# Kernel tuning notes

Measured on AMD Instinct MI355X. Metric: run time of the kernel, lower is better.

Reference implementation:

```python
import jax, jax.numpy as jnp
import numpy as np

GROUP = 5  # in-group size implied by `expected_in = indices.shape[1] * 5`


def setup_inputs() -> dict:
    key = jax.random.key(0)
    k1, k2, k3, k4 = jax.random.split(key, 4)
    T, IN, OUT, G, C, K = 64, 4100, 12288, 820, 2, 256
    x = jax.random.normal(k1, (T, IN), dtype=jnp.float32)
    indices = jax.random.randint(k2, (OUT, G, C), 0, K, dtype=jnp.int32)
    codebooks = (jax.random.normal(k3, (C, K, GROUP), dtype=jnp.float32) * 0.05).astype(jnp.float16)
    scales = jax.random.uniform(k4, (OUT,), dtype=jnp.float32, minval=0.5, maxval=1.5)
    return {"x": x, "indices": indices, "codebooks": codebooks, "scales": scales}


def reference(x, indices, codebooks, scales):
    orig_shape = x.shape
    x_flat = x.reshape(-1, orig_shape[-1])
    expected_in = indices.shape[1] * GROUP
    pad = expected_in - x_flat.shape[1]
    if pad > 0:
        x_flat = jnp.pad(x_flat, ((0, 0), (0, pad)))
    # safety scaling (fp16 overflow guard), as in the torch module
    x_max = jnp.maximum(jnp.abs(x_flat).max(), 1.0) * 8.0
    cb_max = jnp.maximum(jnp.abs(codebooks).astype(jnp.float32).max(), 1.0)
    x_safe = (x_flat / x_max).astype(jnp.float16)
    cb_safe = (codebooks.astype(jnp.float32) / cb_max).astype(jnp.float16)
    # additive-codebook dequant: W[o, g] = sum_c cb_safe[c, indices[o,g,c], :]
    C = cb_safe.shape[0]
    gathered = cb_safe[jnp.arange(C)[None, None, :], indices]  # (O, G, C, GROUP) fp16
    W = gathered.sum(axis=2).reshape(indices.shape[0], -1)     # (O, expected_in) fp16
    out = jnp.einsum('ti,oi->to', x_safe, W, preferred_element_type=jnp.float32)
    out = out * x_max.astype(jnp.float32) * cb_max
    out = out * scales[None, :]
    out = jnp.nan_to_num(out, nan=0.0, posinf=0.0, neginf=0.0)
    return out.reshape(*orig_shape[:-1], -1).astype(x.dtype)
```

## Files before the change

### kernel.cpp

```cpp
#include <hip/hip_runtime.h>
#include <hip/hip_fp16.h>
#include <cstdint>

#define T_DIM 64
#define IN_DIM 4100
#define OUT_DIM 12288
#define G_DIM 820
#define KCODE 256
#define GRP 5
#define KP 6560
#define KB32 205
#define CHUNKS 41
#define CH_G 20
#define KSPLIT 8
#define NBLK 192
#define LDS_STRIDE 168

typedef _Float16 f16x8 __attribute__((ext_vector_type(8)));
typedef float f32x4 __attribute__((ext_vector_type(4)));

__device__ float g_pmax[256];
__device__ float g_cbmax;
__device__ float g_xmax;
__device__ __align__(16) _Float16 g_cbq[2 * KCODE * 8];
__device__ __align__(16) _Float16 g_xA[4 * KB32 * 64 * 8];
__device__ __align__(16) float g_part[KSPLIT * T_DIM * OUT_DIM];

__device__ __forceinline__ float block_reduce_max(float m, float* sm) {
    for (int off = 32; off > 0; off >>= 1)
        m = fmaxf(m, __shfl_down(m, off));
    int tid = threadIdx.x;
    if ((tid & 63) == 0) sm[tid >> 6] = m;
    __syncthreads();
    float r = fmaxf(fmaxf(sm[0], sm[1]), fmaxf(sm[2], sm[3]));
    __syncthreads();
    return r;
}

__global__ void __launch_bounds__(256) k1_absmax_cb(const float* __restrict__ x,
                                                    const void* __restrict__ cbraw) {
    __shared__ float sm[4];
    int tid = threadIdx.x, bid = blockIdx.x;
    float m = 0.f;
    for (int i = bid * 256 + tid; i < T_DIM * IN_DIM; i += 256 * 256)
        m = fmaxf(m, fabsf(x[i]));
    float r = block_reduce_max(m, sm);
    if (tid == 0) g_pmax[bid] = r;

    if (bid == 0) {
        unsigned u0 = *(const unsigned*)cbraw;
        bool is_f32 = (((u0 >> 23) & 0xFF) >= 100);
        float mm = 0.f;
        for (int i = tid; i < 2 * KCODE * GRP; i += 256) {
            float v = is_f32 ? ((const float*)cbraw)[i]
                             : (float)((const _Float16*)cbraw)[i];
            mm = fmaxf(mm, fabsf(v));
        }
        float cbm = fmaxf(block_reduce_max(mm, sm), 1.0f);
        if (tid == 0) g_cbmax = cbm;
        for (int e = tid; e < 2 * KCODE; e += 256) {
            f16x8 v = {};
            #pragma unroll
            for (int j = 0; j < GRP; ++j) {
                float w = is_f32 ? ((const float*)cbraw)[e * GRP + j]
                                 : (float)((const _Float16*)cbraw)[e * GRP + j];
                v[j] = (_Float16)(w / cbm);
            }
            *(f16x8*)&g_cbq[e * 8] = v;
        }
    }
}

__global__ void __launch_bounds__(256) k2_quant(const float* __restrict__ x) {
    __shared__ float sm[4];
    int tid = threadIdx.x;
    float xm = fmaxf(block_reduce_max(g_pmax[tid], sm), 1.0f) * 8.0f;
    if (blockIdx.x == 0 && tid == 0) g_xmax = xm;

    int gt = blockIdx.x * 256 + tid;
    int lane = gt & 63;
    int rest = gt >> 6;
    int kb32 = rest % KB32;
    int t16 = rest / KB32;
    int r16 = lane & 15, q = lane >> 4;
    int t = t16 * 16 + r16;
    int g = kb32 * 4 + q;
    const float* xp = x + (size_t)t * IN_DIM + g * GRP;
    float inv = 1.0f / xm;
    f16x8 v = {};
    #pragma unroll
    for (int j = 0; j < GRP; ++j) v[j] = (_Float16)(xp[j] * inv);
    *(f16x8*)&g_xA[(size_t)gt * 8] = v;
}

__global__ void __launch_bounds__(256) k3_gemm(const int* __restrict__ indices) {
    __shared__ alignas(16) _Float16 w_lds[64 * LDS_STRIDE];
    __shared__ f16x8 cb_sh[2 * KCODE];

    int tid = threadIdx.x;
    int nb = blockIdx.x % NBLK;
    int ksp = blockIdx.x / NBLK;
    int n_base = nb * 64;

    for (int e = tid; e < 2 * KCODE; e += 256)
        cb_sh[e] = *(const f16x8*)&g_cbq[e * 8];

    int sro[5], sgl[5];
    #pragma unroll
    for (int j = 0; j < 5; ++j) {
        int s = tid + j * 256;
        sro[j] = s / 20; sgl[j] = s - sro[j] * 20;
    }

    const int c0 = (CHUNKS * ksp) / KSPLIT;
    const int c1 = (CHUNKS * (ksp + 1)) / KSPLIT;
    const int wid = tid >> 6, lane = tid & 63;
    const int q = lane >> 4, r16 = lane & 15;

    f32x4 acc[4] = {};
    int2 idxr[5];
    uint4 ar[5];
    auto prefetch = [&](int c) {
        int g0 = c * CH_G, kb = c * 5;
        #pragma unroll
        for (int j = 0; j < 5; ++j) {
            ar[j] = *(const uint4*)&g_xA[(size_t)((wid * KB32 + kb + j) * 64 + lane) * 8];
            idxr[j] = *(const int2*)&indices[(size_t)(n_base + sro[j]) * (G_DIM * 2)
                                             + (size_t)(g0 + sgl[j]) * 2];
        }
    };

    prefetch(c0);
    __syncthreads();

    for (int c = c0; c < c1; ++c) {
        #pragma unroll
        for (int j = 0; j < 5; ++j) {
            f16x8 w = cb_sh[idxr[j].x] + cb_sh[KCODE + idxr[j].y];
            *(f16x8*)&w_lds[sro[j] * LDS_STRIDE + sgl[j] * 8] = w;
        }
        uint4 acur[5];
        #pragma unroll
        for (int j = 0; j < 5; ++j) acur[j] = ar[j];
        __syncthreads();
        if (c + 1 < c1) prefetch(c + 1);
        #pragma unroll
        for (int kk = 0; kk < 5; ++kk) {
            f16x8 a = *(f16x8*)&acur[kk];
            #pragma unroll
            for (int nt = 0; nt < 4; ++nt) {
                f16x8 b = *(const f16x8*)&w_lds[(nt * 16 + r16) * LDS_STRIDE + kk * 32 + q * 8];
                acc[nt] = __builtin_amdgcn_mfma_f32_16x16x32_f16(a, b, acc[nt], 0, 0, 0);
            }
        }
        __syncthreads();
    }

    float* pp = g_part + (size_t)ksp * (T_DIM * OUT_DIM);
    #pragma unroll
    for (int nt = 0; nt < 4; ++nt) {
        #pragma unroll
        for (int rr = 0; rr < 4; ++rr) {
            int t = wid * 16 + q * 4 + rr;
            int o = n_base + nt * 16 + r16;
            pp[t * OUT_DIM + o] = acc[nt][rr];
        }
    }
}

__global__ void __launch_bounds__(256) k4_final(const float* __restrict__ scales,
                                                float* __restrict__ out) {
    int i4 = blockIdx.x * 256 + threadIdx.x;
    if (i4 >= T_DIM * OUT_DIM / 4) return;
    float s = g_xmax * g_cbmax;
    const f32x4* p = (const f32x4*)g_part;
    const int Q = T_DIM * OUT_DIM / 4;
    f32x4 v = p[i4];
    #pragma unroll
    for (int k = 1; k < KSPLIT; ++k) v += p[k * Q + i4];
    int o4 = i4 % (OUT_DIM / 4);
    f32x4 sc = *(const f32x4*)&scales[o4 * 4];
    f32x4 r;
    #pragma unroll
    for (int j = 0; j < 4; ++j) {
        float u = v[j] * s * sc[j];
        if (!isfinite(u)) u = 0.f;
        r[j] = u;
    }
    ((f32x4*)out)[i4] = r;
}

extern "C" void kernel_launch(void* const* d_in, const int* in_sizes, int n_in,
                              void* d_out, int out_size, void* d_ws, size_t ws_size,
                              hipStream_t stream) {
    const float* x = (const float*)d_in[0];
    const int* indices = (const int*)d_in[1];
    const void* cbraw = (const void*)d_in[2];
    const float* scales = (const float*)d_in[3];
    float* out = (float*)d_out;
    (void)d_ws; (void)ws_size; (void)n_in; (void)in_sizes; (void)out_size;

    k1_absmax_cb<<<256, 256, 0, stream>>>(x, cbraw);
    k2_quant<<<205, 256, 0, stream>>>(x);
    k3_gemm<<<NBLK * KSPLIT, 256, 0, stream>>>(indices);
    k4_final<<<T_DIM * OUT_DIM / 4 / 256, 256, 0, stream>>>(scales, out);
}
```

Baseline: 153.5 us.

## Merge prep kernels, halve K-split, and remap GEMM warps to N tiles

The absmax and quantization kernels are merged into one launch. Each block now redundantly scans all of x (vectorized float4) to get the global max, and an extra block handles codebook normalization. This removes one launch and the partial-max round trip but adds redundant global reads. In the GEMM, each wave now owns a 16-column N slice and loads all four T tiles of A from global per chunk, so each B fragment from LDS is reused four times. KSPLIT drops from 8 to 4, which halves partial-sum traffic in the final reduction but gives each block more sequential K work, and launch_bounds requests 3 blocks per SM.

```diff
diff --git a/kernel.cpp b/kernel.cpp
--- a/kernel.cpp
+++ b/kernel.cpp
@@ -8,18 +8,16 @@
 #define G_DIM 820
 #define KCODE 256
 #define GRP 5
-#define KP 6560
 #define KB32 205
 #define CHUNKS 41
 #define CH_G 20
-#define KSPLIT 8
+#define KSPLIT 4
 #define NBLK 192
 #define LDS_STRIDE 168
 
 typedef _Float16 f16x8 __attribute__((ext_vector_type(8)));
 typedef float f32x4 __attribute__((ext_vector_type(4)));
 
-__device__ float g_pmax[256];
 __device__ float g_cbmax;
 __device__ float g_xmax;
 __device__ __align__(16) _Float16 g_cbq[2 * KCODE * 8];
@@ -37,17 +35,12 @@
     return r;
 }
 
-__global__ void __launch_bounds__(256) k1_absmax_cb(const float* __restrict__ x,
-                                                    const void* __restrict__ cbraw) {
+__global__ void __launch_bounds__(256) k2_quant(const float* __restrict__ x,
+                                                const void* __restrict__ cbraw) {
     __shared__ float sm[4];
     int tid = threadIdx.x, bid = blockIdx.x;
-    float m = 0.f;
-    for (int i = bid * 256 + tid; i < T_DIM * IN_DIM; i += 256 * 256)
-        m = fmaxf(m, fabsf(x[i]));
-    float r = block_reduce_max(m, sm);
-    if (tid == 0) g_pmax[bid] = r;
-
-    if (bid == 0) {
+
+    if (bid == 205) {
         unsigned u0 = *(const unsigned*)cbraw;
         bool is_f32 = (((u0 >> 23) & 0xFF) >= 100);
         float mm = 0.f;
@@ -68,23 +61,26 @@
             }
             *(f16x8*)&g_cbq[e * 8] = v;
         }
-    }
-}
-
-__global__ void __launch_bounds__(256) k2_quant(const float* __restrict__ x) {
-    __shared__ float sm[4];
-    int tid = threadIdx.x;
-    float xm = fmaxf(block_reduce_max(g_pmax[tid], sm), 1.0f) * 8.0f;
-    if (blockIdx.x == 0 && tid == 0) g_xmax = xm;
-
-    int gt = blockIdx.x * 256 + tid;
+        return;
+    }
+
+    float m = 0.f;
+    const f32x4* x4 = (const f32x4*)x;
+    for (int i = tid; i < T_DIM * IN_DIM / 4; i += 256) {
+        f32x4 v = x4[i];
+        m = fmaxf(m, fmaxf(fmaxf(fabsf(v[0]), fabsf(v[1])),
+                           fmaxf(fabsf(v[2]), fabsf(v[3]))));
+    }
+    float xm = fmaxf(block_reduce_max(m, sm), 1.0f) * 8.0f;
+    if (bid == 0 && tid == 0) g_xmax = xm;
+
+    int gt = bid * 256 + tid;
     int lane = gt & 63;
     int rest = gt >> 6;
     int kb32 = rest % KB32;
     int t16 = rest / KB32;
-    int r16 = lane & 15, q = lane >> 4;
-    int t = t16 * 16 + r16;
-    int g = kb32 * 4 + q;
+    int t = t16 * 16 + (lane & 15);
+    int g = kb32 * 4 + (lane >> 4);
     const float* xp = x + (size_t)t * IN_DIM + g * GRP;
     float inv = 1.0f / xm;
     f16x8 v = {};
@@ -93,7 +89,7 @@
     *(f16x8*)&g_xA[(size_t)gt * 8] = v;
 }
 
-__global__ void __launch_bounds__(256) k3_gemm(const int* __restrict__ indices) {
+__global__ void __launch_bounds__(256, 3) k3_gemm(const int* __restrict__ indices) {
     __shared__ alignas(16) _Float16 w_lds[64 * LDS_STRIDE];
     __shared__ f16x8 cb_sh[2 * KCODE];
 
@@ -119,18 +115,15 @@
 
     f32x4 acc[4] = {};
     int2 idxr[5];
-    uint4 ar[5];
-    auto prefetch = [&](int c) {
-        int g0 = c * CH_G, kb = c * 5;
-        #pragma unroll
-        for (int j = 0; j < 5; ++j) {
-            ar[j] = *(const uint4*)&g_xA[(size_t)((wid * KB32 + kb + j) * 64 + lane) * 8];
+    auto pref_idx = [&](int c) {
+        int g0 = c * CH_G;
+        #pragma unroll
+        for (int j = 0; j < 5; ++j)
             idxr[j] = *(const int2*)&indices[(size_t)(n_base + sro[j]) * (G_DIM * 2)
                                              + (size_t)(g0 + sgl[j]) * 2];
-        }
     };
 
-    prefetch(c0);
+    pref_idx(c0);
     __syncthreads();
 
     for (int c = c0; c < c1; ++c) {
@@ -139,31 +132,34 @@
             f16x8 w = cb_sh[idxr[j].x] + cb_sh[KCODE + idxr[j].y];
             *(f16x8*)&w_lds[sro[j] * LDS_STRIDE + sgl[j] * 8] = w;
         }
-        uint4 acur[5];
-        #pragma unroll
-        for (int j = 0; j < 5; ++j) acur[j] = ar[j];
+        uint4 ar20[20];
+        #pragma unroll
+        for (int t16 = 0; t16 < 4; ++t16)
+            #pragma unroll
+            for (int kk = 0; kk < 5; ++kk)
+                ar20[t16 * 5 + kk] = *(const uint4*)
+                    &g_xA[(size_t)((t16 * KB32 + c * 5 + kk) * 64 + lane) * 8];
         __syncthreads();
-        if (c + 1 < c1) prefetch(c + 1);
+        if (c + 1 < c1) pref_idx(c + 1);
         #pragma unroll
         for (int kk = 0; kk < 5; ++kk) {
-            f16x8 a = *(f16x8*)&acur[kk];
+            f16x8 b = *(const f16x8*)&w_lds[(wid * 16 + r16) * LDS_STRIDE + kk * 32 + q * 8];
             #pragma unroll
-            for (int nt = 0; nt < 4; ++nt) {
-                f16x8 b = *(const f16x8*)&w_lds[(nt * 16 + r16) * LDS_STRIDE + kk * 32 + q * 8];
-                acc[nt] = __builtin_amdgcn_mfma_f32_16x16x32_f16(a, b, acc[nt], 0, 0, 0);
-            }
+            for (int t16 = 0; t16 < 4; ++t16)
+                acc[t16] = __builtin_amdgcn_mfma_f32_16x16x32_f16(
+                    *(f16x8*)&ar20[t16 * 5 + kk], b, acc[t16], 0, 0, 0);
         }
         __syncthreads();
     }
 
     float* pp = g_part + (size_t)ksp * (T_DIM * OUT_DIM);
-    #pragma unroll
-    for (int nt = 0; nt < 4; ++nt) {
+    int o = n_base + wid * 16 + r16;
+    #pragma unroll
+    for (int t16 = 0; t16 < 4; ++t16) {
         #pragma unroll
         for (int rr = 0; rr < 4; ++rr) {
-            int t = wid * 16 + q * 4 + rr;
-            int o = n_base + nt * 16 + r16;
-            pp[t * OUT_DIM + o] = acc[nt][rr];
+            int t = t16 * 16 + q * 4 + rr;
+            pp[t * OUT_DIM + o] = acc[t16][rr];
         }
     }
 }
@@ -200,8 +196,7 @@
     float* out = (float*)d_out;
     (void)d_ws; (void)ws_size; (void)n_in; (void)in_sizes; (void)out_size;
 
-    k1_absmax_cb<<<256, 256, 0, stream>>>(x, cbraw);
-    k2_quant<<<205, 256, 0, stream>>>(x);
+    k2_quant<<<206, 256, 0, stream>>>(x, cbraw);
     k3_gemm<<<NBLK * KSPLIT, 256, 0, stream>>>(indices);
     k4_final<<<T_DIM * OUT_DIM / 4 / 256, 256, 0, stream>>>(scales, out);
 }
```

Measured after the change: 234.2 us. +52.6%, slower.
